# Performance work log

Hardware: AMD Instinct MI355X
Metric: run time of the kernel (lower is better)

The kernel has to match this reference:

```python
import jax, jax.numpy as jnp
from jax import lax
import numpy as np

B, P, N = 4, 12000, 100   # batch, max_pillars, max_points_per_pillar
H, W = 108, 124           # pseudo-image size from forward()
DN = ('NCHW', 'HWIO', 'NCHW')


def _conv(x, k, b):
    y = lax.conv_general_dilated(x, k, (1, 1), 'SAME', dimension_numbers=DN)
    return y + b[None, :, None, None]


def _cbr(x, k, b, s, t):
    # Conv2d + folded BatchNorm2d (eval: per-channel scale/shift) + ReLU
    y = _conv(x, k, b)
    return jax.nn.relu(y * s[None, :, None, None] + t[None, :, None, None])


def _pool(x):
    return lax.reduce_window(x, -jnp.inf, lax.max, (1, 1, 2, 2), (1, 1, 2, 2), 'VALID')


def setup_inputs() -> dict:
    key = jax.random.key(0)
    ks = iter(jax.random.split(key, 64))
    d = {}
    d['pillars'] = jax.random.normal(next(ks), (B, P, N, 9), jnp.float32)

    def w(shape, scale=0.05):
        return jax.random.normal(next(ks), shape, jnp.float32) * scale

    d['w1'] = w((9, 64)); d['b1'] = w((64,))
    d['s1'] = 1.0 + w((64,)); d['t1'] = w((64,))
    d['w2'] = w((64, 64)); d['b2'] = w((64,))
    d['s2'] = 1.0 + w((64,)); d['t2'] = w((64,))
    chans = [(64, 64), (64, 64), (64, 128), (128, 128), (128, 256), (256, 256)]
    for i, (ci, co) in enumerate(chans, 1):
        d['ck%d' % i] = w((3, 3, ci, co)); d['cb%d' % i] = w((co,))
        d['cs%d' % i] = 1.0 + w((co,)); d['ct%d' % i] = w((co,))
    d['hk1'] = w((3, 3, 256, 256)); d['hb1'] = w((256,))
    d['hk2'] = w((1, 1, 256, 10)); d['hb2'] = w((10,))
    d['num_points'] = jax.random.randint(next(ks), (B, P), 0, 100, jnp.int32)
    return d


def reference(pillars, w1, b1, s1, t1, w2, b2, s2, t2,
              ck1, cb1, cs1, ct1, ck2, cb2, cs2, ct2,
              ck3, cb3, cs3, ct3, ck4, cb4, cs4, ct4,
              ck5, cb5, cs5, ct5, ck6, cb6, cs6, ct6,
              hk1, hb1, hk2, hb2, num_points):
    # pillar feature net: Linear+BN(folded)+ReLU x2, batched over all points  [B,P,N,9] -> [B,P,N,64]
    h = jax.nn.relu((pillars @ w1 + b1) * s1 + t1)
    h = jax.nn.relu((h @ w2 + b2) * s2 + t2)
    # masked segment-max over the variable-length point groups
    mask = jnp.arange(N)[None, None, :] < num_points[:, :, None]          # [B,P,N]
    neg = jnp.finfo(h.dtype).min
    feat = jnp.max(jnp.where(mask[..., None], h, neg), axis=2)            # [B,P,64]
    valid = num_points > 0
    feat = jnp.where(valid[..., None], feat, 0.0)
    cnt = jnp.maximum(jnp.sum(valid, axis=1), 1).astype(feat.dtype)       # [B]
    mean = jnp.sum(feat, axis=1) / cnt[:, None]                           # [B,64]
    # nearest-interpolate a 1x1 map to HxW == broadcast
    x = jnp.broadcast_to(mean[:, :, None, None], (pillars.shape[0], 64, H, W))
    # 2D backbone
    x = _cbr(x, ck1, cb1, cs1, ct1); x = _cbr(x, ck2, cb2, cs2, ct2); x = _pool(x)
    x = _cbr(x, ck3, cb3, cs3, ct3); x = _cbr(x, ck4, cb4, cs4, ct4); x = _pool(x)
    x = _cbr(x, ck5, cb5, cs5, ct5); x = _cbr(x, ck6, cb6, cs6, ct6)
    # detection head
    y = jax.nn.relu(_conv(x, hk1, hb1))
    return _conv(y, hk2, hb2)   # [B, num_classes+7=10, 27, 31]
```

## Files before the change

### kernel.cpp

```cpp
#include <hip/hip_runtime.h>

typedef __bf16 vbf8 __attribute__((ext_vector_type(8)));
typedef unsigned short us8 __attribute__((ext_vector_type(8)));
typedef float f32x4 __attribute__((ext_vector_type(4)));
typedef float f32x4u __attribute__((ext_vector_type(4), aligned(4)));

__device__ __forceinline__ int caseof(int h, int H, int e) {
  if (h < 0 || h >= H) return -1;
  if (h < e) return h;
  if (h >= H - e) return h - (H - 1) + 2 * e;
  return e;
}
__device__ __forceinline__ int repof(int i, int H, int eo) {
  return (i <= eo) ? i : H - 1 - 2 * eo + i;
}

__device__ __forceinline__ vbf8 max8(vbf8 a, vbf8 b) {
  us8 ua = __builtin_bit_cast(us8, a), ub = __builtin_bit_cast(us8, b);
  us8 o;
#pragma unroll
  for (int e = 0; e < 8; ++e) o[e] = ua[e] > ub[e] ? ua[e] : ub[e];
  return __builtin_bit_cast(vbf8, o);
}

__global__ void setup_kernel(const float* __restrict__ w1, const float* __restrict__ b1,
                             const float* __restrict__ s1, const float* __restrict__ t1,
                             const float* __restrict__ w2, const float* __restrict__ b2,
                             const float* __restrict__ s2, const float* __restrict__ t2,
                             __bf16* __restrict__ wfrag, float* __restrict__ be2f) {
  int l = threadIdx.x;
  int s = l & 15, g = l >> 4;
#pragma unroll
  for (int m = 0; m < 4; ++m) {
    int c = 32 * (m & 1) + 8 * (s >> 2) + 4 * (m >> 1) + (s & 3);
#pragma unroll
    for (int e = 0; e < 8; ++e) {
      int k = g * 8 + e;
      float v = 0.f;
      if (k < 9)       v = w1[k * 64 + c] * s1[c];
      else if (k == 9) v = fmaf(b1[c], s1[c], t1[c]);
      wfrag[(m * 64 + l) * 8 + e] = (__bf16)v;
    }
    int co = s + 16 * m;
#pragma unroll
    for (int e = 0; e < 8; ++e) {
      int k = g * 8 + e;
      wfrag[((4 + m) * 64 + l) * 8 + e] = (__bf16)(w2[k * 64 + co] * s2[co]);
      wfrag[((8 + m) * 64 + l) * 8 + e] = (__bf16)(w2[(32 + k) * 64 + co] * s2[co]);
    }
    be2f[m * 64 + l] = fmaf(b2[co], s2[co], t2[co]);
  }
}

__global__ __launch_bounds__(256) void convw_kernel(
    const float* __restrict__ k1, const float* __restrict__ k2,
    const float* __restrict__ k3, const float* __restrict__ k4,
    const float* __restrict__ k5, const float* __restrict__ k6,
    const float* __restrict__ kh, __bf16* __restrict__ wT) {
  __shared__ float tile[64][65];
  const int tCI[7]    = {64, 64, 64, 128, 128, 256, 256};
  const int tCO[7]    = {64, 64, 128, 128, 256, 256, 256};
  const int tOFF[7]   = {0, 36864, 73728, 147456, 294912, 589824, 1179648};
  const int tTILES[7] = {9, 9, 18, 36, 72, 144, 144};
  int bid = blockIdx.x;
  int ti = 0, acc = 0;
  while (ti < 6 && bid >= acc + tTILES[ti]) { acc += tTILES[ti]; ++ti; }
  int lt = bid - acc;
  int CI = tCI[ti], CO = tCO[ti];
  const float* src;
  if (ti == 0) src = k1; else if (ti == 1) src = k2; else if (ti == 2) src = k3;
  else if (ti == 3) src = k4; else if (ti == 4) src = k5; else if (ti == 5) src = k6;
  else src = kh;
  int cot = CO / 64, tpt = (CI / 64) * cot;
  int tap = lt / tpt; int r2 = lt - tap * tpt;
  int ci0 = (r2 / cot) * 64, co0 = (r2 % cot) * 64;
  const float* sp = src + (size_t)(tap * CI + ci0) * CO + co0;
  int t = threadIdx.x;
  int lr = t >> 6, lc = t & 63;
#pragma unroll
  for (int rr = 0; rr < 64; rr += 4)
    tile[rr + lr][lc] = sp[(size_t)(rr + lr) * CO + lc];
  __syncthreads();
  __bf16* dst = wT + tOFF[ti] + ((size_t)tap * CO + co0) * CI + ci0;
#pragma unroll
  for (int rr = 0; rr < 64; rr += 4)
    dst[(size_t)(rr + lr) * CI + lc] = (__bf16)tile[lc][rr + lr];
}

__global__ __launch_bounds__(256) void pillar_kernel(
    const float* __restrict__ pil, const int* __restrict__ npt,
    const __bf16* __restrict__ wfrag, const float* __restrict__ be2f,
    float* __restrict__ partial, int* __restrict__ pcnt)
{
  __shared__ float redf[4][64];
  __shared__ int redc[4];
  const int tid = threadIdx.x;
  const int wv = tid >> 6, lane = tid & 63;
  const int s = lane & 15, g = lane >> 4;
  const int wid = blockIdx.x * 4 + wv;
  const int b = wid / 6000;
  const int p0 = (wid - b * 6000) * 2;

  vbf8 w1f[4], w2f0[4], w2f1[4];
  float be2[4];
#pragma unroll
  for (int m = 0; m < 4; ++m) {
    w1f[m]  = *(const vbf8*)(wfrag + ((0 + m) * 64 + lane) * 8);
    w2f0[m] = *(const vbf8*)(wfrag + ((4 + m) * 64 + lane) * 8);
    w2f1[m] = *(const vbf8*)(wfrag + ((8 + m) * 64 + lane) * 8);
    be2[m] = be2f[m * 64 + lane];
  }

  float fsum[4] = {0.f, 0.f, 0.f, 0.f};
  int cnt = 0;

  for (int i = 0; i < 2; ++i) {
    int pidx = b * 12000 + p0 + i;
    int np = npt[pidx];
    if (np <= 0) continue;
    ++cnt;
    float feat[4][4];
#pragma unroll
    for (int n = 0; n < 4; ++n)
#pragma unroll
      for (int r = 0; r < 4; ++r) feat[n][r] = 0.f;

    int ngrp = (np + 15) >> 4;
    const float* pbase = pil + (size_t)pidx * 900;
    const float* pp0 = pbase + s * 9;
    f32x4u lo = *(const f32x4u*)pp0;
    f32x4u hi = *(const f32x4u*)(pp0 + 4);
    float v8 = pp0[8];
    for (int grp = 0; grp < ngrp; ++grp) {
      int g2 = min(grp + 1, ngrp - 1);
      int ptn = min(g2 * 16 + s, 99);
      const float* ppn = pbase + ptn * 9;
      f32x4u nlo = *(const f32x4u*)ppn;
      f32x4u nhi = *(const f32x4u*)(ppn + 4);
      float nv8 = ppn[8];

      vbf8 b1f;
      b1f[0] = (__bf16)(g == 0 ? lo[0] : (g == 1 ? v8 : 0.f));
      b1f[1] = (__bf16)(g == 0 ? lo[1] : (g == 1 ? 1.0f : 0.f));
      b1f[2] = (__bf16)(g == 0 ? lo[2] : 0.f);
      b1f[3] = (__bf16)(g == 0 ? lo[3] : 0.f);
      b1f[4] = (__bf16)(g == 0 ? hi[0] : 0.f);
      b1f[5] = (__bf16)(g == 0 ? hi[1] : 0.f);
      b1f[6] = (__bf16)(g == 0 ? hi[2] : 0.f);
      b1f[7] = (__bf16)(g == 0 ? hi[3] : 0.f);

      const f32x4 z = {0.f, 0.f, 0.f, 0.f};
      f32x4 d1[4];
#pragma unroll
      for (int m = 0; m < 4; ++m)
        d1[m] = __builtin_amdgcn_mfma_f32_16x16x32_bf16(w1f[m], b1f, z, 0, 0, 0);

      vbf8 a2f0, a2f1;
#pragma unroll
      for (int r = 0; r < 4; ++r) {
        a2f0[r]     = (__bf16)fmaxf(d1[0][r], 0.f);
        a2f1[r]     = (__bf16)fmaxf(d1[1][r], 0.f);
        a2f0[4 + r] = (__bf16)fmaxf(d1[2][r], 0.f);
        a2f1[4 + r] = (__bf16)fmaxf(d1[3][r], 0.f);
      }

      f32x4 d2[4];
#pragma unroll
      for (int n = 0; n < 4; ++n) {
        f32x4 cb = {be2[n], be2[n], be2[n], be2[n]};
        d2[n] = __builtin_amdgcn_mfma_f32_16x16x32_bf16(a2f0, w2f0[n], cb, 0, 0, 0);
        d2[n] = __builtin_amdgcn_mfma_f32_16x16x32_bf16(a2f1, w2f1[n], d2[n], 0, 0, 0);
      }
      if (((grp + 1) << 4) <= np) {
#pragma unroll
        for (int n = 0; n < 4; ++n)
#pragma unroll
          for (int r = 0; r < 4; ++r) feat[n][r] = fmaxf(feat[n][r], d2[n][r]);
      } else {
#pragma unroll
        for (int n = 0; n < 4; ++n)
#pragma unroll
          for (int r = 0; r < 4; ++r) {
            float vv = (grp * 16 + 4 * g + r < np) ? d2[n][r] : 0.f;
            feat[n][r] = fmaxf(feat[n][r], vv);
          }
      }
      lo = nlo; hi = nhi; v8 = nv8;
    }
#pragma unroll
    for (int n = 0; n < 4; ++n) {
      float m = fmaxf(fmaxf(feat[n][0], feat[n][1]), fmaxf(feat[n][2], feat[n][3]));
      m = fmaxf(m, __shfl_xor(m, 16));
      m = fmaxf(m, __shfl_xor(m, 32));
      fsum[n] += m;
    }
  }
  if (g == 0) {
#pragma unroll
    for (int n = 0; n < 4; ++n) redf[wv][s + 16 * n] = fsum[n];
  }
  if (lane == 0) redc[wv] = cnt;
  __syncthreads();
  if (tid < 64) {
    float tot = redf[0][tid] + redf[1][tid] + redf[2][tid] + redf[3][tid];
    partial[blockIdx.x * 64 + tid] = tot;
    if (tid == 0) pcnt[blockIdx.x] = redc[0] + redc[1] + redc[2] + redc[3];
  }
}

__global__ void mean_kernel(const float* __restrict__ partial,
                            const int* __restrict__ pcnt,
                            __bf16* __restrict__ x0, __bf16* __restrict__ zbuf) {
  int b = blockIdx.x, t = threadIdx.x;
  if (b == 0) zbuf[t] = (__bf16)0.f;
  int c = t & 63, q = t >> 6;
  float sum = 0.f;
  for (int w = q; w < 1500; w += 4) sum += partial[(b * 1500 + w) * 64 + c];
  int cl = 0;
  for (int w = t; w < 1500; w += 256) cl += pcnt[b * 1500 + w];
  __shared__ float sh[256];
  __shared__ int shc[256];
  sh[t] = sum; shc[t] = cl;
  __syncthreads();
  for (int o = 128; o > 0; o >>= 1) {
    if (t < o) shc[t] += shc[t + o];
    __syncthreads();
  }
  if (t < 64) {
    float tot = sh[t] + sh[t + 64] + sh[t + 128] + sh[t + 192];
    x0[b * 64 + t] = (__bf16)(tot / (float)(shc[0] > 0 ? shc[0] : 1));
  }
}

template <int CI, int CO, int H, int EIN, bool POOL, bool HAS_BN, bool OUT_F32>
__global__ __launch_bounds__(256) void caseconv_kernel(
    const __bf16* __restrict__ xin, const __bf16* __restrict__ wt,
    const float* __restrict__ cb, const float* __restrict__ cs,
    const float* __restrict__ ct, __bf16* __restrict__ yout,
    float* __restrict__ yf32, const __bf16* __restrict__ zbuf)
{
  constexpr int EV   = POOL ? (EIN + 1) / 2 : EIN;
  constexpr int EOUT = EV + 1;
  constexpr int NBI  = 2 * EIN + 1;
  constexpr int HX   = POOL ? 2 * H : H;
  constexpr int NBO  = 2 * EOUT + 1;
  constexpr int M    = NBO * NBO * 4;
  constexpr int NT   = CO / 16;
  constexpr int KC   = CI / 32;
  constexpr int MT   = (M + 31) / 32;
  const int wid = blockIdx.x * 4 + (threadIdx.x >> 6);
  if (wid >= MT * NT) return;
  const int lane = threadIdx.x & 63;
  const int s = lane & 15, g = lane >> 4;
  const int nt = wid % NT, mt = wid / NT;

  int reph[2], repw[2], bsel[2];
#pragma unroll
  for (int mf = 0; mf < 2; ++mf) {
    int m = mt * 32 + mf * 16 + s; if (m >= M) m = M - 1;
    bsel[mf] = m & 3; int q = m >> 2;
    int bw = q % NBO, bh = q / NBO;
    reph[mf] = repof(bh, H, EOUT); repw[mf] = repof(bw, H, EOUT);
  }

  f32x4 acc0 = {0.f, 0.f, 0.f, 0.f}, acc1 = {0.f, 0.f, 0.f, 0.f};
#pragma unroll
  for (int tap = 0; tap < 9; ++tap) {
    const int dh = tap / 3, dw = tap % 3;
    const __bf16* wtap = wt + ((size_t)tap * CO + nt * 16) * CI + 8 * g;
    const __bf16* base[2][POOL ? 4 : 1];
#pragma unroll
    for (int mf = 0; mf < 2; ++mf) {
      int vh = reph[mf] + dh - 1, vw = repw[mf] + dw - 1;
      if constexpr (POOL) {
        bool valid = (vh >= 0) && (vh < H) && (vw >= 0) && (vw < H);
        int h0 = 0, h1 = 0, w0 = 0, w1 = 0;
        if (valid) {
          h0 = caseof(2 * vh, HX, EIN); h1 = caseof(2 * vh + 1, HX, EIN);
          w0 = caseof(2 * vw, HX, EIN); w1 = caseof(2 * vw + 1, HX, EIN);
        }
        base[mf][0] = valid ? xin + (size_t)((h0 * NBI + w0) * 4 + bsel[mf]) * CI : zbuf;
        base[mf][1] = valid ? xin + (size_t)((h0 * NBI + w1) * 4 + bsel[mf]) * CI : zbuf;
        base[mf][2] = valid ? xin + (size_t)((h1 * NBI + w0) * 4 + bsel[mf]) * CI : zbuf;
        base[mf][3] = valid ? xin + (size_t)((h1 * NBI + w1) * 4 + bsel[mf]) * CI : zbuf;
      } else {
        int jh = caseof(vh, H, EIN), jw = caseof(vw, H, EIN);
        bool v = (jh >= 0) && (jw >= 0);
        base[mf][0] = v ? xin + (size_t)((jh * NBI + jw) * 4 + bsel[mf]) * CI : zbuf;
      }
    }
#pragma unroll
    for (int ck = 0; ck < KC; ++ck) {
      vbf8 a0, a1;
      if constexpr (POOL) {
        a0 = max8(max8(*(const vbf8*)(base[0][0] + ck * 32 + 8 * g),
                       *(const vbf8*)(base[0][1] + ck * 32 + 8 * g)),
                  max8(*(const vbf8*)(base[0][2] + ck * 32 + 8 * g),
                       *(const vbf8*)(base[0][3] + ck * 32 + 8 * g)));
        a1 = max8(max8(*(const vbf8*)(base[1][0] + ck * 32 + 8 * g),
                       *(const vbf8*)(base[1][1] + ck * 32 + 8 * g)),
                  max8(*(const vbf8*)(base[1][2] + ck * 32 + 8 * g),
                       *(const vbf8*)(base[1][3] + ck * 32 + 8 * g)));
      } else {
        a0 = *(const vbf8*)(base[0][0] + ck * 32 + 8 * g);
        a1 = *(const vbf8*)(base[1][0] + ck * 32 + 8 * g);
      }
      vbf8 bb = *(const vbf8*)(wtap + (size_t)s * CI + ck * 32);
      acc0 = __builtin_amdgcn_mfma_f32_16x16x32_bf16(a0, bb, acc0, 0, 0, 0);
      acc1 = __builtin_amdgcn_mfma_f32_16x16x32_bf16(a1, bb, acc1, 0, 0, 0);
    }
  }

  int co = nt * 16 + s;
  float sc, sh;
  if (HAS_BN) { sc = cs[co]; sh = fmaf(cb[co], sc, ct[co]); }
  else        { sc = 1.f;    sh = cb[co]; }
#pragma unroll
  for (int mf = 0; mf < 2; ++mf) {
    f32x4 acc = mf ? acc1 : acc0;
#pragma unroll
    for (int r = 0; r < 4; ++r) {
      int m = mt * 32 + mf * 16 + 4 * g + r;
      if (m < M) {
        float v = fmaxf(fmaf(acc[r], sc, sh), 0.f);
        if constexpr (OUT_F32) yf32[(size_t)m * CO + co] = v;
        else                   yout[(size_t)m * CO + co] = (__bf16)v;
      }
    }
  }
}

__global__ void headscatter_kernel(const float* __restrict__ x,
                                   const float* __restrict__ wk,
                                   const float* __restrict__ bias,
                                   float* __restrict__ out) {
  int idx = blockIdx.x * 256 + threadIdx.x;
  if (idx >= 4 * 10 * 27 * 31) return;
  int c = idx % 31;
  int r = (idx / 31) % 27;
  int ch = (idx / (31 * 27)) % 10;
  int b = idx / (31 * 27 * 10);
  int rr = (r <= 7) ? r : ((r >= 20) ? r - 11 : 7);
  int cc = (c <= 7) ? c : ((c >= 24) ? c - 15 : 7);
  int ph = caseof(rr, 16, 5), pw = caseof(cc, 16, 5);
  const float* xr = x + (size_t)((ph * 11 + pw) * 4 + b) * 256;
  float a0 = 0.f, a1 = 0.f, a2 = 0.f, a3 = 0.f;
#pragma unroll 4
  for (int ci = 0; ci < 256; ci += 4) {
    float4 in4 = *(const float4*)(xr + ci);
    a0 = fmaf(in4.x, wk[(ci + 0) * 10 + ch], a0);
    a1 = fmaf(in4.y, wk[(ci + 1) * 10 + ch], a1);
    a2 = fmaf(in4.z, wk[(ci + 2) * 10 + ch], a2);
    a3 = fmaf(in4.w, wk[(ci + 3) * 10 + ch], a3);
  }
  out[idx] = (a0 + a1) + (a2 + a3) + bias[ch];
}

extern "C" void kernel_launch(void* const* d_in, const int* in_sizes, int n_in,
                              void* d_out, int out_size, void* d_ws, size_t ws_size,
                              hipStream_t stream) {
  (void)in_sizes; (void)n_in; (void)out_size; (void)ws_size;
  const float* pillars = (const float*)d_in[0];
  const float* w1 = (const float*)d_in[1];
  const float* b1 = (const float*)d_in[2];
  const float* s1 = (const float*)d_in[3];
  const float* t1 = (const float*)d_in[4];
  const float* w2 = (const float*)d_in[5];
  const float* b2 = (const float*)d_in[6];
  const float* s2 = (const float*)d_in[7];
  const float* t2 = (const float*)d_in[8];
  const float* ck[6], *cbv[6], *csv[6], *ctv[6];
  for (int i = 0; i < 6; ++i) {
    ck[i]  = (const float*)d_in[9 + i * 4];
    cbv[i] = (const float*)d_in[10 + i * 4];
    csv[i] = (const float*)d_in[11 + i * 4];
    ctv[i] = (const float*)d_in[12 + i * 4];
  }
  const float* hk1 = (const float*)d_in[33];
  const float* hb1 = (const float*)d_in[34];
  const float* hk2 = (const float*)d_in[35];
  const float* hb2 = (const float*)d_in[36];
  const int* num_points = (const int*)d_in[37];
  float* out = (float*)d_out;

  char* wsb = (char*)d_ws;
  size_t off = 0;
  auto alloc = [&](size_t n) { char* p = wsb + off; off = (off + n + 255) & ~(size_t)255; return p; };
  float*  ppart = (float*)alloc(1536000);
  int*    pcnt  = (int*)alloc(24000);
  __bf16* wfrag = (__bf16*)alloc(12288);
  float*  be2f  = (float*)alloc(1024);
  __bf16* wT    = (__bf16*)alloc(3538944);
  __bf16* zbuf  = (__bf16*)alloc(512);
  __bf16* X0    = (__bf16*)alloc(512);
  __bf16* X1    = (__bf16*)alloc(4608);
  __bf16* X2    = (__bf16*)alloc(12800);
  __bf16* X3    = (__bf16*)alloc(25600);
  __bf16* X4    = (__bf16*)alloc(50176);
  __bf16* X5    = (__bf16*)alloc(100352);
  __bf16* X6    = (__bf16*)alloc(165888);
  float*  XH    = (float*)alloc(495616);

  __bf16* wt1 = wT + 0;       __bf16* wt2 = wT + 36864;
  __bf16* wt3 = wT + 73728;   __bf16* wt4 = wT + 147456;
  __bf16* wt5 = wT + 294912;  __bf16* wt6 = wT + 589824;
  __bf16* wth = wT + 1179648;

  setup_kernel<<<1, 64, 0, stream>>>(w1, b1, s1, t1, w2, b2, s2, t2, wfrag, be2f);
  convw_kernel<<<432, 256, 0, stream>>>(ck[0], ck[1], ck[2], ck[3], ck[4], ck[5],
                                        hk1, wT);
  pillar_kernel<<<6000, 256, 0, stream>>>(pillars, num_points, wfrag, be2f,
                                          ppart, pcnt);
  mean_kernel<<<4, 256, 0, stream>>>(ppart, pcnt, X0, zbuf);

  caseconv_kernel<64, 64, 64, 0, false, true, false><<<2, 256, 0, stream>>>(
      X0, wt1, cbv[0], csv[0], ctv[0], X1, nullptr, zbuf);
  caseconv_kernel<64, 64, 64, 1, false, true, false><<<4, 256, 0, stream>>>(
      X1, wt2, cbv[1], csv[1], ctv[1], X2, nullptr, zbuf);
  caseconv_kernel<64, 128, 32, 2, true, true, false><<<8, 256, 0, stream>>>(
      X2, wt3, cbv[2], csv[2], ctv[2], X3, nullptr, zbuf);
  caseconv_kernel<128, 128, 32, 2, false, true, false><<<14, 256, 0, stream>>>(
      X3, wt4, cbv[3], csv[3], ctv[3], X4, nullptr, zbuf);
  caseconv_kernel<128, 256, 16, 3, true, true, false><<<28, 256, 0, stream>>>(
      X4, wt5, cbv[4], csv[4], ctv[4], X5, nullptr, zbuf);
  caseconv_kernel<256, 256, 16, 3, false, true, false><<<44, 256, 0, stream>>>(
      X5, wt6, cbv[5], csv[5], ctv[5], X6, nullptr, zbuf);
  caseconv_kernel<256, 256, 16, 4, false, false, true><<<64, 256, 0, stream>>>(
      X6, wth, hb1, nullptr, nullptr, nullptr, XH, zbuf);
  headscatter_kernel<<<131, 256, 0, stream>>>(XH, hk2, hb2, out);
}
```

Before: 363.3 us.

## Fuse weight prep into pillar kernel and whole backbone into one per-batch kernel

The weight transpose and MLP weight folding now run inside the pillar kernel: the first 432 blocks do the conv-weight transposes, and every wave builds its MLP fragments directly from the fp32 parameters instead of loading them from a setup buffer. The mean reduction, all six backbone convs, the head conv and the 1x1 head scatter are merged into one kernel with one 1024-thread block per batch, keeping activations in LDS. This removes about ten kernel launches and the global round-trips between layers. In exchange each backbone stage runs on only 4 blocks, which leaves most CUs idle, and every pillar wave repeats the scalar weight folding.

```diff
diff --git a/kernel.cpp b/kernel.cpp
--- a/kernel.cpp
+++ b/kernel.cpp
@@ -23,13 +23,56 @@
   return __builtin_bit_cast(vbf8, o);
 }
 
-__global__ void setup_kernel(const float* __restrict__ w1, const float* __restrict__ b1,
-                             const float* __restrict__ s1, const float* __restrict__ t1,
-                             const float* __restrict__ w2, const float* __restrict__ b2,
-                             const float* __restrict__ s2, const float* __restrict__ t2,
-                             __bf16* __restrict__ wfrag, float* __restrict__ be2f) {
-  int l = threadIdx.x;
-  int s = l & 15, g = l >> 4;
+__global__ __launch_bounds__(256) void pillar_kernel(
+    const float* __restrict__ pil, const int* __restrict__ npt,
+    const float* __restrict__ w1, const float* __restrict__ b1,
+    const float* __restrict__ s1, const float* __restrict__ t1,
+    const float* __restrict__ w2, const float* __restrict__ b2,
+    const float* __restrict__ s2, const float* __restrict__ t2,
+    const float* __restrict__ k1, const float* __restrict__ k2,
+    const float* __restrict__ k3, const float* __restrict__ k4,
+    const float* __restrict__ k5, const float* __restrict__ k6,
+    const float* __restrict__ kh, __bf16* __restrict__ wT,
+    float* __restrict__ partial, int* __restrict__ pcnt)
+{
+  __shared__ float tile[64][65];
+  __shared__ float redf[4][64];
+  __shared__ int redc[4];
+  const int tid = threadIdx.x;
+  const int wv = tid >> 6, lane = tid & 63;
+  const int s = lane & 15, g = lane >> 4;
+
+  if (blockIdx.x < 432) {
+    const int tCI[7]    = {64, 64, 64, 128, 128, 256, 256};
+    const int tCO[7]    = {64, 64, 128, 128, 256, 256, 256};
+    const int tOFF[7]   = {0, 36864, 73728, 147456, 294912, 589824, 1179648};
+    const int tTILES[7] = {9, 9, 18, 36, 72, 144, 144};
+    int bid = blockIdx.x;
+    int ti = 0, acc = 0;
+    while (ti < 6 && bid >= acc + tTILES[ti]) { acc += tTILES[ti]; ++ti; }
+    int lt = bid - acc;
+    int CI = tCI[ti], CO = tCO[ti];
+    const float* src;
+    if (ti == 0) src = k1; else if (ti == 1) src = k2; else if (ti == 2) src = k3;
+    else if (ti == 3) src = k4; else if (ti == 4) src = k5; else if (ti == 5) src = k6;
+    else src = kh;
+    int cot = CO / 64, tpt = (CI / 64) * cot;
+    int tap = lt / tpt; int r2 = lt - tap * tpt;
+    int ci0 = (r2 / cot) * 64, co0 = (r2 % cot) * 64;
+    const float* sp = src + (size_t)(tap * CI + ci0) * CO + co0;
+    int lr = tid >> 6, lc = tid & 63;
+#pragma unroll
+    for (int rr = 0; rr < 64; rr += 4)
+      tile[rr + lr][lc] = sp[(size_t)(rr + lr) * CO + lc];
+    __syncthreads();
+    __bf16* dst = wT + tOFF[ti] + ((size_t)tap * CO + co0) * CI + ci0;
+#pragma unroll
+    for (int rr = 0; rr < 64; rr += 4)
+      dst[(size_t)(rr + lr) * CI + lc] = (__bf16)tile[lc][rr + lr];
+  }
+
+  vbf8 w1f[4], w2f0[4], w2f1[4];
+  float be2[4];
 #pragma unroll
   for (int m = 0; m < 4; ++m) {
     int c = 32 * (m & 1) + 8 * (s >> 2) + 4 * (m >> 1) + (s & 3);
@@ -39,77 +82,21 @@
       float v = 0.f;
       if (k < 9)       v = w1[k * 64 + c] * s1[c];
       else if (k == 9) v = fmaf(b1[c], s1[c], t1[c]);
-      wfrag[(m * 64 + l) * 8 + e] = (__bf16)v;
+      w1f[m][e] = (__bf16)v;
     }
     int co = s + 16 * m;
 #pragma unroll
     for (int e = 0; e < 8; ++e) {
       int k = g * 8 + e;
-      wfrag[((4 + m) * 64 + l) * 8 + e] = (__bf16)(w2[k * 64 + co] * s2[co]);
-      wfrag[((8 + m) * 64 + l) * 8 + e] = (__bf16)(w2[(32 + k) * 64 + co] * s2[co]);
-    }
-    be2f[m * 64 + l] = fmaf(b2[co], s2[co], t2[co]);
-  }
-}
-
-__global__ __launch_bounds__(256) void convw_kernel(
-    const float* __restrict__ k1, const float* __restrict__ k2,
-    const float* __restrict__ k3, const float* __restrict__ k4,
-    const float* __restrict__ k5, const float* __restrict__ k6,
-    const float* __restrict__ kh, __bf16* __restrict__ wT) {
-  __shared__ float tile[64][65];
-  const int tCI[7]    = {64, 64, 64, 128, 128, 256, 256};
-  const int tCO[7]    = {64, 64, 128, 128, 256, 256, 256};
-  const int tOFF[7]   = {0, 36864, 73728, 147456, 294912, 589824, 1179648};
-  const int tTILES[7] = {9, 9, 18, 36, 72, 144, 144};
-  int bid = blockIdx.x;
-  int ti = 0, acc = 0;
-  while (ti < 6 && bid >= acc + tTILES[ti]) { acc += tTILES[ti]; ++ti; }
-  int lt = bid - acc;
-  int CI = tCI[ti], CO = tCO[ti];
-  const float* src;
-  if (ti == 0) src = k1; else if (ti == 1) src = k2; else if (ti == 2) src = k3;
-  else if (ti == 3) src = k4; else if (ti == 4) src = k5; else if (ti == 5) src = k6;
-  else src = kh;
-  int cot = CO / 64, tpt = (CI / 64) * cot;
-  int tap = lt / tpt; int r2 = lt - tap * tpt;
-  int ci0 = (r2 / cot) * 64, co0 = (r2 % cot) * 64;
-  const float* sp = src + (size_t)(tap * CI + ci0) * CO + co0;
-  int t = threadIdx.x;
-  int lr = t >> 6, lc = t & 63;
-#pragma unroll
-  for (int rr = 0; rr < 64; rr += 4)
-    tile[rr + lr][lc] = sp[(size_t)(rr + lr) * CO + lc];
-  __syncthreads();
-  __bf16* dst = wT + tOFF[ti] + ((size_t)tap * CO + co0) * CI + ci0;
-#pragma unroll
-  for (int rr = 0; rr < 64; rr += 4)
-    dst[(size_t)(rr + lr) * CI + lc] = (__bf16)tile[lc][rr + lr];
-}
-
-__global__ __launch_bounds__(256) void pillar_kernel(
-    const float* __restrict__ pil, const int* __restrict__ npt,
-    const __bf16* __restrict__ wfrag, const float* __restrict__ be2f,
-    float* __restrict__ partial, int* __restrict__ pcnt)
-{
-  __shared__ float redf[4][64];
-  __shared__ int redc[4];
-  const int tid = threadIdx.x;
-  const int wv = tid >> 6, lane = tid & 63;
-  const int s = lane & 15, g = lane >> 4;
+      w2f0[m][e] = (__bf16)(w2[k * 64 + co] * s2[co]);
+      w2f1[m][e] = (__bf16)(w2[(32 + k) * 64 + co] * s2[co]);
+    }
+    be2[m] = fmaf(b2[co], s2[co], t2[co]);
+  }
+
   const int wid = blockIdx.x * 4 + wv;
   const int b = wid / 6000;
   const int p0 = (wid - b * 6000) * 2;
-
-  vbf8 w1f[4], w2f0[4], w2f1[4];
-  float be2[4];
-#pragma unroll
-  for (int m = 0; m < 4; ++m) {
-    w1f[m]  = *(const vbf8*)(wfrag + ((0 + m) * 64 + lane) * 8);
-    w2f0[m] = *(const vbf8*)(wfrag + ((4 + m) * 64 + lane) * 8);
-    w2f1[m] = *(const vbf8*)(wfrag + ((8 + m) * 64 + lane) * 8);
-    be2[m] = be2f[m * 64 + lane];
-  }
 
   float fsum[4] = {0.f, 0.f, 0.f, 0.f};
   int cnt = 0;
@@ -208,152 +195,196 @@
   }
 }
 
-__global__ void mean_kernel(const float* __restrict__ partial,
-                            const int* __restrict__ pcnt,
-                            __bf16* __restrict__ x0, __bf16* __restrict__ zbuf) {
-  int b = blockIdx.x, t = threadIdx.x;
-  if (b == 0) zbuf[t] = (__bf16)0.f;
-  int c = t & 63, q = t >> 6;
-  float sum = 0.f;
-  for (int w = q; w < 1500; w += 4) sum += partial[(b * 1500 + w) * 64 + c];
-  int cl = 0;
-  for (int w = t; w < 1500; w += 256) cl += pcnt[b * 1500 + w];
-  __shared__ float sh[256];
-  __shared__ int shc[256];
-  sh[t] = sum; shc[t] = cl;
-  __syncthreads();
-  for (int o = 128; o > 0; o >>= 1) {
-    if (t < o) shc[t] += shc[t + o];
-    __syncthreads();
-  }
-  if (t < 64) {
-    float tot = sh[t] + sh[t + 64] + sh[t + 128] + sh[t + 192];
-    x0[b * 64 + t] = (__bf16)(tot / (float)(shc[0] > 0 ? shc[0] : 1));
-  }
-}
-
 template <int CI, int CO, int H, int EIN, bool POOL, bool HAS_BN, bool OUT_F32>
-__global__ __launch_bounds__(256) void caseconv_kernel(
-    const __bf16* __restrict__ xin, const __bf16* __restrict__ wt,
+__device__ __forceinline__ void caseconvL(
+    int wv, int lane, const __bf16* __restrict__ xin,
+    const __bf16* __restrict__ wt,
     const float* __restrict__ cb, const float* __restrict__ cs,
-    const float* __restrict__ ct, __bf16* __restrict__ yout,
-    float* __restrict__ yf32, const __bf16* __restrict__ zbuf)
+    const float* __restrict__ ct,
+    __bf16* __restrict__ yout, float* __restrict__ yf32,
+    const __bf16* __restrict__ zpad, int m0, int mcount)
 {
   constexpr int EV   = POOL ? (EIN + 1) / 2 : EIN;
   constexpr int EOUT = EV + 1;
   constexpr int NBI  = 2 * EIN + 1;
   constexpr int HX   = POOL ? 2 * H : H;
   constexpr int NBO  = 2 * EOUT + 1;
-  constexpr int M    = NBO * NBO * 4;
   constexpr int NT   = CO / 16;
   constexpr int KC   = CI / 32;
-  constexpr int MT   = (M + 31) / 32;
-  const int wid = blockIdx.x * 4 + (threadIdx.x >> 6);
-  if (wid >= MT * NT) return;
-  const int lane = threadIdx.x & 63;
   const int s = lane & 15, g = lane >> 4;
-  const int nt = wid % NT, mt = wid / NT;
-
-  int reph[2], repw[2], bsel[2];
-#pragma unroll
-  for (int mf = 0; mf < 2; ++mf) {
-    int m = mt * 32 + mf * 16 + s; if (m >= M) m = M - 1;
-    bsel[mf] = m & 3; int q = m >> 2;
-    int bw = q % NBO, bh = q / NBO;
-    reph[mf] = repof(bh, H, EOUT); repw[mf] = repof(bw, H, EOUT);
-  }
-
-  f32x4 acc0 = {0.f, 0.f, 0.f, 0.f}, acc1 = {0.f, 0.f, 0.f, 0.f};
-#pragma unroll
-  for (int tap = 0; tap < 9; ++tap) {
-    const int dh = tap / 3, dw = tap % 3;
-    const __bf16* wtap = wt + ((size_t)tap * CO + nt * 16) * CI + 8 * g;
-    const __bf16* base[2][POOL ? 4 : 1];
+  const int MT = (mcount + 31) >> 5;
+  for (int wid = wv; wid < MT * NT; wid += 16) {
+    const int nt = wid % NT, mt = wid / NT;
+    int reph[2], repw[2];
 #pragma unroll
     for (int mf = 0; mf < 2; ++mf) {
-      int vh = reph[mf] + dh - 1, vw = repw[mf] + dw - 1;
-      if constexpr (POOL) {
-        bool valid = (vh >= 0) && (vh < H) && (vw >= 0) && (vw < H);
-        int h0 = 0, h1 = 0, w0 = 0, w1 = 0;
-        if (valid) {
-          h0 = caseof(2 * vh, HX, EIN); h1 = caseof(2 * vh + 1, HX, EIN);
-          w0 = caseof(2 * vw, HX, EIN); w1 = caseof(2 * vw + 1, HX, EIN);
+      int m = m0 + mt * 32 + mf * 16 + s;
+      if (m >= m0 + mcount) m = m0 + mcount - 1;
+      int bh = m / NBO, bw = m % NBO;
+      reph[mf] = repof(bh, H, EOUT); repw[mf] = repof(bw, H, EOUT);
+    }
+    f32x4 acc0 = {0.f, 0.f, 0.f, 0.f}, acc1 = {0.f, 0.f, 0.f, 0.f};
+#pragma unroll
+    for (int tap = 0; tap < 9; ++tap) {
+      const int dh = tap / 3, dw = tap % 3;
+      const __bf16* wtap = wt + ((size_t)tap * CO + nt * 16) * CI + 8 * g;
+      const __bf16* base[2][POOL ? 4 : 1];
+#pragma unroll
+      for (int mf = 0; mf < 2; ++mf) {
+        int vh = reph[mf] + dh - 1, vw = repw[mf] + dw - 1;
+        if constexpr (POOL) {
+          bool valid = (vh >= 0) && (vh < H) && (vw >= 0) && (vw < H);
+          int h0 = 0, h1 = 0, w0 = 0, w1 = 0;
+          if (valid) {
+            h0 = caseof(2 * vh, HX, EIN); h1 = caseof(2 * vh + 1, HX, EIN);
+            w0 = caseof(2 * vw, HX, EIN); w1 = caseof(2 * vw + 1, HX, EIN);
+          }
+          base[mf][0] = valid ? xin + (size_t)(h0 * NBI + w0) * CI : zpad;
+          base[mf][1] = valid ? xin + (size_t)(h0 * NBI + w1) * CI : zpad;
+          base[mf][2] = valid ? xin + (size_t)(h1 * NBI + w0) * CI : zpad;
+          base[mf][3] = valid ? xin + (size_t)(h1 * NBI + w1) * CI : zpad;
+        } else {
+          int jh = caseof(vh, H, EIN), jw = caseof(vw, H, EIN);
+          bool v = (jh >= 0) && (jw >= 0);
+          base[mf][0] = v ? xin + (size_t)(jh * NBI + jw) * CI : zpad;
         }
-        base[mf][0] = valid ? xin + (size_t)((h0 * NBI + w0) * 4 + bsel[mf]) * CI : zbuf;
-        base[mf][1] = valid ? xin + (size_t)((h0 * NBI + w1) * 4 + bsel[mf]) * CI : zbuf;
-        base[mf][2] = valid ? xin + (size_t)((h1 * NBI + w0) * 4 + bsel[mf]) * CI : zbuf;
-        base[mf][3] = valid ? xin + (size_t)((h1 * NBI + w1) * 4 + bsel[mf]) * CI : zbuf;
-      } else {
-        int jh = caseof(vh, H, EIN), jw = caseof(vw, H, EIN);
-        bool v = (jh >= 0) && (jw >= 0);
-        base[mf][0] = v ? xin + (size_t)((jh * NBI + jw) * 4 + bsel[mf]) * CI : zbuf;
-      }
-    }
-#pragma unroll
-    for (int ck = 0; ck < KC; ++ck) {
-      vbf8 a0, a1;
-      if constexpr (POOL) {
-        a0 = max8(max8(*(const vbf8*)(base[0][0] + ck * 32 + 8 * g),
-                       *(const vbf8*)(base[0][1] + ck * 32 + 8 * g)),
-                  max8(*(const vbf8*)(base[0][2] + ck * 32 + 8 * g),
-                       *(const vbf8*)(base[0][3] + ck * 32 + 8 * g)));
-        a1 = max8(max8(*(const vbf8*)(base[1][0] + ck * 32 + 8 * g),
-                       *(const vbf8*)(base[1][1] + ck * 32 + 8 * g)),
-                  max8(*(const vbf8*)(base[1][2] + ck * 32 + 8 * g),
-                       *(const vbf8*)(base[1][3] + ck * 32 + 8 * g)));
-      } else {
-        a0 = *(const vbf8*)(base[0][0] + ck * 32 + 8 * g);
-        a1 = *(const vbf8*)(base[1][0] + ck * 32 + 8 * g);
-      }
-      vbf8 bb = *(const vbf8*)(wtap + (size_t)s * CI + ck * 32);
-      acc0 = __builtin_amdgcn_mfma_f32_16x16x32_bf16(a0, bb, acc0, 0, 0, 0);
-      acc1 = __builtin_amdgcn_mfma_f32_16x16x32_bf16(a1, bb, acc1, 0, 0, 0);
-    }
-  }
-
-  int co = nt * 16 + s;
-  float sc, sh;
-  if (HAS_BN) { sc = cs[co]; sh = fmaf(cb[co], sc, ct[co]); }
-  else        { sc = 1.f;    sh = cb[co]; }
-#pragma unroll
-  for (int mf = 0; mf < 2; ++mf) {
-    f32x4 acc = mf ? acc1 : acc0;
-#pragma unroll
-    for (int r = 0; r < 4; ++r) {
-      int m = mt * 32 + mf * 16 + 4 * g + r;
-      if (m < M) {
-        float v = fmaxf(fmaf(acc[r], sc, sh), 0.f);
-        if constexpr (OUT_F32) yf32[(size_t)m * CO + co] = v;
-        else                   yout[(size_t)m * CO + co] = (__bf16)v;
-      }
-    }
-  }
-}
-
-__global__ void headscatter_kernel(const float* __restrict__ x,
-                                   const float* __restrict__ wk,
-                                   const float* __restrict__ bias,
-                                   float* __restrict__ out) {
-  int idx = blockIdx.x * 256 + threadIdx.x;
-  if (idx >= 4 * 10 * 27 * 31) return;
-  int c = idx % 31;
-  int r = (idx / 31) % 27;
-  int ch = (idx / (31 * 27)) % 10;
-  int b = idx / (31 * 27 * 10);
-  int rr = (r <= 7) ? r : ((r >= 20) ? r - 11 : 7);
-  int cc = (c <= 7) ? c : ((c >= 24) ? c - 15 : 7);
-  int ph = caseof(rr, 16, 5), pw = caseof(cc, 16, 5);
-  const float* xr = x + (size_t)((ph * 11 + pw) * 4 + b) * 256;
-  float a0 = 0.f, a1 = 0.f, a2 = 0.f, a3 = 0.f;
+      }
+#pragma unroll
+      for (int ck = 0; ck < KC; ++ck) {
+        vbf8 a0, a1;
+        if constexpr (POOL) {
+          a0 = max8(max8(*(const vbf8*)(base[0][0] + ck * 32 + 8 * g),
+                         *(const vbf8*)(base[0][1] + ck * 32 + 8 * g)),
+                    max8(*(const vbf8*)(base[0][2] + ck * 32 + 8 * g),
+                         *(const vbf8*)(base[0][3] + ck * 32 + 8 * g)));
+          a1 = max8(max8(*(const vbf8*)(base[1][0] + ck * 32 + 8 * g),
+                         *(const vbf8*)(base[1][1] + ck * 32 + 8 * g)),
+                    max8(*(const vbf8*)(base[1][2] + ck * 32 + 8 * g),
+                         *(const vbf8*)(base[1][3] + ck * 32 + 8 * g)));
+        } else {
+          a0 = *(const vbf8*)(base[0][0] + ck * 32 + 8 * g);
+          a1 = *(const vbf8*)(base[1][0] + ck * 32 + 8 * g);
+        }
+        vbf8 bb = *(const vbf8*)(wtap + (size_t)s * CI + ck * 32);
+        acc0 = __builtin_amdgcn_mfma_f32_16x16x32_bf16(a0, bb, acc0, 0, 0, 0);
+        acc1 = __builtin_amdgcn_mfma_f32_16x16x32_bf16(a1, bb, acc1, 0, 0, 0);
+      }
+    }
+    int co = nt * 16 + s;
+    float sc, sh;
+    if (HAS_BN) { sc = cs[co]; sh = fmaf(cb[co], sc, ct[co]); }
+    else        { sc = 1.f;    sh = cb[co]; }
+#pragma unroll
+    for (int mf = 0; mf < 2; ++mf) {
+      f32x4 acc = mf ? acc1 : acc0;
+#pragma unroll
+      for (int r = 0; r < 4; ++r) {
+        int m = m0 + mt * 32 + mf * 16 + 4 * g + r;
+        if (m < m0 + mcount) {
+          float v = fmaxf(fmaf(acc[r], sc, sh), 0.f);
+          if constexpr (OUT_F32) yf32[(size_t)(m - m0) * CO + co] = v;
+          else                   yout[(size_t)m * CO + co] = (__bf16)v;
+        }
+      }
+    }
+  }
+}
+
+__global__ __launch_bounds__(1024) void backbone_kernel(
+    const float* __restrict__ ppart, const int* __restrict__ pcnt,
+    const __bf16* wt1, const __bf16* wt2, const __bf16* wt3, const __bf16* wt4,
+    const __bf16* wt5, const __bf16* wt6, const __bf16* wth,
+    const float* cb1, const float* cs1, const float* ct1,
+    const float* cb2, const float* cs2, const float* ct2,
+    const float* cb3, const float* cs3, const float* ct3,
+    const float* cb4, const float* cs4, const float* ct4,
+    const float* cb5, const float* cs5, const float* ct5,
+    const float* cb6, const float* cs6, const float* ct6,
+    const float* hb1, const float* hk2, const float* hb2,
+    float* __restrict__ out)
+{
+  __shared__ float Af[64 * 256];
+  __shared__ __bf16 Bb[81 * 256];
+  __shared__ __bf16 X0l[64];
+  __shared__ __bf16 zpad[256];
+  const int tid = threadIdx.x;
+  const int wv = tid >> 6, lane = tid & 63;
+  const int b = blockIdx.x;
+
+  {
+    int c = tid & 63, q = tid >> 6;
+    float sum = 0.f;
+    for (int w = q; w < 1500; w += 16) sum += ppart[(b * 1500 + w) * 64 + c];
+    int cl = 0;
+    for (int w = tid; w < 1500; w += 1024) cl += pcnt[b * 1500 + w];
+    Af[tid] = sum;
+    int* shi = (int*)Bb;
+    shi[tid] = cl;
+    __syncthreads();
+    for (int o = 512; o > 0; o >>= 1) {
+      if (tid < o) shi[tid] += shi[tid + o];
+      __syncthreads();
+    }
+    if (tid < 64) {
+      float tot = 0.f;
+#pragma unroll
+      for (int q2 = 0; q2 < 16; ++q2) tot += Af[q2 * 64 + tid];
+      X0l[tid] = (__bf16)(tot / (float)(shi[0] > 0 ? shi[0] : 1));
+    }
+    if (tid < 256) zpad[tid] = (__bf16)0.f;
+    __syncthreads();
+  }
+  __bf16* A16 = (__bf16*)Af;
+
+  caseconvL<64, 64, 64, 0, false, true, false>(wv, lane, X0l, wt1, cb1, cs1, ct1,
+                                               A16, nullptr, zpad, 0, 9);
+  __syncthreads();
+  caseconvL<64, 64, 64, 1, false, true, false>(wv, lane, A16, wt2, cb2, cs2, ct2,
+                                               Bb, nullptr, zpad, 0, 25);
+  __syncthreads();
+  caseconvL<64, 128, 32, 2, true, true, false>(wv, lane, Bb, wt3, cb3, cs3, ct3,
+                                               A16, nullptr, zpad, 0, 25);
+  __syncthreads();
+  caseconvL<128, 128, 32, 2, false, true, false>(wv, lane, A16, wt4, cb4, cs4, ct4,
+                                                 Bb, nullptr, zpad, 0, 49);
+  __syncthreads();
+  caseconvL<128, 256, 16, 3, true, true, false>(wv, lane, Bb, wt5, cb5, cs5, ct5,
+                                                A16, nullptr, zpad, 0, 49);
+  __syncthreads();
+  caseconvL<256, 256, 16, 3, false, true, false>(wv, lane, A16, wt6, cb6, cs6, ct6,
+                                                 Bb, nullptr, zpad, 0, 81);
+  __syncthreads();
+
+  for (int chunk = 0; chunk < 2; ++chunk) {
+    int m0 = chunk * 64, mc = chunk ? 57 : 64;
+    caseconvL<256, 256, 16, 4, false, false, true>(wv, lane, Bb, wth, hb1,
+                                                   nullptr, nullptr, nullptr,
+                                                   Af, zpad, m0, mc);
+    __syncthreads();
+    for (int t = tid; t < 8370; t += 1024) {
+      int ch = t / 837, rc = t % 837;
+      int r = rc / 31, c = rc % 31;
+      int rr = (r <= 7) ? r : ((r >= 20) ? r - 11 : 7);
+      int cc = (c <= 7) ? c : ((c >= 24) ? c - 15 : 7);
+      int ph = caseof(rr, 16, 5), pw = caseof(cc, 16, 5);
+      int m = ph * 11 + pw;
+      if (m >= m0 && m < m0 + mc) {
+        const float* xr = Af + (size_t)(m - m0) * 256;
+        float a0 = 0.f, a1 = 0.f, a2 = 0.f, a3 = 0.f;
 #pragma unroll 4
-  for (int ci = 0; ci < 256; ci += 4) {
-    float4 in4 = *(const float4*)(xr + ci);
-    a0 = fmaf(in4.x, wk[(ci + 0) * 10 + ch], a0);
-    a1 = fmaf(in4.y, wk[(ci + 1) * 10 + ch], a1);
-    a2 = fmaf(in4.z, wk[(ci + 2) * 10 + ch], a2);
-    a3 = fmaf(in4.w, wk[(ci + 3) * 10 + ch], a3);
-  }
-  out[idx] = (a0 + a1) + (a2 + a3) + bias[ch];
+        for (int ci = 0; ci < 256; ci += 4) {
+          float4 in4 = *(const float4*)(xr + ci);
+          a0 = fmaf(in4.x, hk2[(ci + 0) * 10 + ch], a0);
+          a1 = fmaf(in4.y, hk2[(ci + 1) * 10 + ch], a1);
+          a2 = fmaf(in4.z, hk2[(ci + 2) * 10 + ch], a2);
+          a3 = fmaf(in4.w, hk2[(ci + 3) * 10 + ch], a3);
+        }
+        out[((size_t)(b * 10 + ch) * 27 + r) * 31 + c] =
+            (a0 + a1) + (a2 + a3) + hb2[ch];
+      }
+    }
+    __syncthreads();
+  }
 }
 
 extern "C" void kernel_launch(void* const* d_in, const int* in_sizes, int n_in,
@@ -388,44 +419,20 @@
   auto alloc = [&](size_t n) { char* p = wsb + off; off = (off + n + 255) & ~(size_t)255; return p; };
   float*  ppart = (float*)alloc(1536000);
   int*    pcnt  = (int*)alloc(24000);
-  __bf16* wfrag = (__bf16*)alloc(12288);
-  float*  be2f  = (float*)alloc(1024);
   __bf16* wT    = (__bf16*)alloc(3538944);
-  __bf16* zbuf  = (__bf16*)alloc(512);
-  __bf16* X0    = (__bf16*)alloc(512);
-  __bf16* X1    = (__bf16*)alloc(4608);
-  __bf16* X2    = (__bf16*)alloc(12800);
-  __bf16* X3    = (__bf16*)alloc(25600);
-  __bf16* X4    = (__bf16*)alloc(50176);
-  __bf16* X5    = (__bf16*)alloc(100352);
-  __bf16* X6    = (__bf16*)alloc(165888);
-  float*  XH    = (float*)alloc(495616);
 
   __bf16* wt1 = wT + 0;       __bf16* wt2 = wT + 36864;
   __bf16* wt3 = wT + 73728;   __bf16* wt4 = wT + 147456;
   __bf16* wt5 = wT + 294912;  __bf16* wt6 = wT + 589824;
   __bf16* wth = wT + 1179648;
 
-  setup_kernel<<<1, 64, 0, stream>>>(w1, b1, s1, t1, w2, b2, s2, t2, wfrag, be2f);
-  convw_kernel<<<432, 256, 0, stream>>>(ck[0], ck[1], ck[2], ck[3], ck[4], ck[5],
-                                        hk1, wT);
-  pillar_kernel<<<6000, 256, 0, stream>>>(pillars, num_points, wfrag, be2f,
-                                          ppart, pcnt);
-  mean_kernel<<<4, 256, 0, stream>>>(ppart, pcnt, X0, zbuf);
-
-  caseconv_kernel<64, 64, 64, 0, false, true, false><<<2, 256, 0, stream>>>(
-      X0, wt1, cbv[0], csv[0], ctv[0], X1, nullptr, zbuf);
-  caseconv_kernel<64, 64, 64, 1, false, true, false><<<4, 256, 0, stream>>>(
-      X1, wt2, cbv[1], csv[1], ctv[1], X2, nullptr, zbuf);
-  caseconv_kernel<64, 128, 32, 2, true, true, false><<<8, 256, 0, stream>>>(
-      X2, wt3, cbv[2], csv[2], ctv[2], X3, nullptr, zbuf);
-  caseconv_kernel<128, 128, 32, 2, false, true, false><<<14, 256, 0, stream>>>(
-      X3, wt4, cbv[3], csv[3], ctv[3], X4, nullptr, zbuf);
-  caseconv_kernel<128, 256, 16, 3, true, true, false><<<28, 256, 0, stream>>>(
-      X4, wt5, cbv[4], csv[4], ctv[4], X5, nullptr, zbuf);
-  caseconv_kernel<256, 256, 16, 3, false, true, false><<<44, 256, 0, stream>>>(
-      X5, wt6, cbv[5], csv[5], ctv[5], X6, nullptr, zbuf);
-  caseconv_kernel<256, 256, 16, 4, false, false, true><<<64, 256, 0, stream>>>(
-      X6, wth, hb1, nullptr, nullptr, nullptr, XH, zbuf);
-  headscatter_kernel<<<131, 256, 0, stream>>>(XH, hk2, hb2, out);
-}
+  pillar_kernel<<<6000, 256, 0, stream>>>(
+      pillars, num_points, w1, b1, s1, t1, w2, b2, s2, t2,
+      ck[0], ck[1], ck[2], ck[3], ck[4], ck[5], hk1, wT, ppart, pcnt);
+  backbone_kernel<<<4, 1024, 0, stream>>>(
+      ppart, pcnt, wt1, wt2, wt3, wt4, wt5, wt6, wth,
+      cbv[0], csv[0], ctv[0], cbv[1], csv[1], ctv[1],
+      cbv[2], csv[2], ctv[2], cbv[3], csv[3], ctv[3],
+      cbv[4], csv[4], ctv[4], cbv[5], csv[5], ctv[5],
+      hb1, hk2, hb2, out);
+}
```

After: 812.6 us. +123.7%, slower.
